# Kernel tuning notes

Hardware: AMD Instinct MI355X
Metric: run time of the kernel (lower is better)

The kernel has to match this reference:

```python
import jax, jax.numpy as jnp
import numpy as np

B, N, F_IN, F_OUT = 8, 2048, 64, 64
ALPHA = 0.2  # LeakyReLU negative slope


def setup_inputs() -> dict:
    key = jax.random.key(0)
    k_in, k_adj, k_w, k_a1, k_a2 = jax.random.split(key, 5)
    inp = jax.random.normal(k_in, (B, N, F_IN), dtype=jnp.float32)
    adj = (jax.random.uniform(k_adj, (B, N, N)) < 0.05).astype(jnp.float32)
    # xavier_uniform with gain=sqrt(2)
    def xavier(k, shape):
        fan_in, fan_out = shape[0], shape[1]
        bound = np.sqrt(2.0) * np.sqrt(6.0 / (fan_in + fan_out))
        return jax.random.uniform(k, shape, jnp.float32, -bound, bound)
    W = xavier(k_w, (F_IN, F_OUT))
    a1 = xavier(k_a1, (F_OUT, 1))
    a2 = xavier(k_a2, (F_OUT, 1))
    bias = jnp.full((N, F_OUT), 0.1, dtype=jnp.float32)
    return {"input": inp, "adj": adj, "W": W, "a1": a1, "a2": a2, "bias": bias}


def reference(input, adj, W, a1, a2, bias):
    # h: [B, N, F_OUT]
    h = jnp.einsum("bnf,fo->bno", input, W)
    f1 = h @ a1          # [B, N, 1]
    f2 = h @ a2          # [B, N, 1]
    e = jax.nn.leaky_relu(f1 + jnp.swapaxes(f2, 1, 2), negative_slope=ALPHA)  # [B, N, N]
    # NOTE: original multiplies adj elementwise (not -inf mask) and softmaxes over dim=1
    attention = jax.nn.softmax(adj * e, axis=1)
    h_prime = jnp.einsum("bij,bjo->bio", attention, h) + bias  # bias broadcasts over batch
    h_prime = h_prime + input  # in_features == out_features, no downsample
    return jax.nn.elu(h_prime)
```

## Files before the change

### kernel.cpp

```cpp
#include <hip/hip_runtime.h>
#include <cstdint>
#include <cstddef>

#define Bn 8
#define Nn 2048
#define Fn 64
#define ALPHA 0.2f

typedef __attribute__((ext_vector_type(8))) short  s8frag;
typedef __attribute__((ext_vector_type(4))) float  f4frag;

__device__ __forceinline__ float lrelu(float x) { return fmaxf(x, ALPHA * x); }
__device__ __forceinline__ float elu(float x)   { return x > 0.f ? x : __expf(x) - 1.f; }
__device__ __forceinline__ unsigned short bfr(float f) {
    unsigned u = __float_as_uint(f);
    u += 0x7fffu + ((u >> 16) & 1u);
    return (unsigned short)(u >> 16);
}

__global__ __launch_bounds__(256) void k1_h_f(
        const float* __restrict__ inp, const float* __restrict__ W,
        const float* __restrict__ a1, const float* __restrict__ a2,
        float* __restrict__ h, float* __restrict__ f1, float* __restrict__ f2) {
    __shared__ float Wl[Fn * Fn];
    __shared__ float inr[4 * Fn];
    int t = threadIdx.x;
    for (int k = t; k < Fn * Fn; k += 256) Wl[k] = W[k];
    size_t row0 = (size_t)blockIdx.x * 4;
    inr[t] = inp[row0 * Fn + t];
    __syncthreads();
    int r = t >> 6, o = t & 63;
    const float* irow = &inr[r * Fn];
    float acc = 0.f;
#pragma unroll
    for (int f = 0; f < Fn; ++f) acc = fmaf(irow[f], Wl[f * Fn + o], acc);
    size_t row = row0 + r;
    h[row * Fn + o] = acc;
    float p = acc * a1[o];
    float q = acc * a2[o];
#pragma unroll
    for (int off = 32; off > 0; off >>= 1) {
        p += __shfl_down(p, off, 64);
        q += __shfl_down(q, off, 64);
    }
    if (o == 0) { f1[row] = p; f2[row] = q; }
}

__global__ __launch_bounds__(256) void k1b_max(
        const float* __restrict__ f1, float* __restrict__ f1max) {
    int b = blockIdx.x, t = threadIdx.x;
    float m = -3.4e38f;
    for (int i = t; i < Nn; i += 256) m = fmaxf(m, f1[b * Nn + i]);
#pragma unroll
    for (int off = 32; off > 0; off >>= 1) m = fmaxf(m, __shfl_down(m, off, 64));
    __shared__ float sm[4];
    if ((t & 63) == 0) sm[t >> 6] = m;
    __syncthreads();
    if (t == 0) f1max[b] = fmaxf(fmaxf(sm[0], sm[1]), fmaxf(sm[2], sm[3]));
}

__global__ __launch_bounds__(512) void k2a_bits(
        const float* __restrict__ adj, const float* __restrict__ f1,
        const float* __restrict__ f2, const float* __restrict__ f1max_p,
        float* __restrict__ Dsum, unsigned char* __restrict__ bitsL) {
    int b = blockIdx.x;
    int cj = blockIdx.y;
    int j0 = cj * 256;
    int i0 = blockIdx.z * 128;
    int w = threadIdx.x >> 6, lane = threadIdx.x & 63;
    float f1max = f1max_p[b];
    float4 f2v = *(const float4*)&f2[b * Nn + j0 + 4 * lane];
    float Mf0 = fmaxf(lrelu(f1max + f2v.x), 0.f);
    float Mf1 = fmaxf(lrelu(f1max + f2v.y), 0.f);
    float Mf2 = fmaxf(lrelu(f1max + f2v.z), 0.f);
    float Mf3 = fmaxf(lrelu(f1max + f2v.w), 0.f);
    float s0 = 0.f, s1 = 0.f, s2 = 0.f, s3 = 0.f;
    const float* abase = adj + ((size_t)b * Nn) * Nn + j0 + 4 * lane;
    const float* f1b = f1 + b * Nn;
    int g = lane >> 1;
    int boff = (g & 3) * 8 + (g >> 2);
    bool evenlane = (lane & 1) == 0;
    size_t bbase = ((size_t)(b * 8 + cj) * Nn) * 32;

    for (int gi = 0; gi < 4; ++gi) {
        int r0 = i0 + w + 32 * gi;
        float4 av0 = *(const float4*)(abase + (size_t)(r0 +  0) * Nn);
        float4 av1 = *(const float4*)(abase + (size_t)(r0 +  8) * Nn);
        float4 av2 = *(const float4*)(abase + (size_t)(r0 + 16) * Nn);
        float4 av3 = *(const float4*)(abase + (size_t)(r0 + 24) * Nn);
        float fi0 = f1b[r0], fi1 = f1b[r0 + 8], fi2 = f1b[r0 + 16], fi3 = f1b[r0 + 24];
#define PROC(AV, FI, IROW)                                                     \
        {                                                                      \
            bool n0 = AV.x != 0.f, n1 = AV.y != 0.f,                           \
                 n2 = AV.z != 0.f, n3 = AV.w != 0.f;                           \
            s0 += __expf((n0 ? lrelu((FI) + f2v.x) : 0.f) - Mf0);              \
            s1 += __expf((n1 ? lrelu((FI) + f2v.y) : 0.f) - Mf1);              \
            s2 += __expf((n2 ? lrelu((FI) + f2v.z) : 0.f) - Mf2);              \
            s3 += __expf((n3 ? lrelu((FI) + f2v.w) : 0.f) - Mf3);              \
            unsigned nib = (unsigned)n0 | ((unsigned)n1 << 1) |                \
                           ((unsigned)n2 << 2) | ((unsigned)n3 << 3);          \
            unsigned other = __shfl_xor(nib, 1, 64);                           \
            if (evenlane)                                                      \
                bitsL[bbase + (size_t)(IROW) * 32 + boff] =                    \
                    (unsigned char)(nib | (other << 4));                       \
        }
        PROC(av0, fi0, r0 +  0)
        PROC(av1, fi1, r0 +  8)
        PROC(av2, fi2, r0 + 16)
        PROC(av3, fi3, r0 + 24)
#undef PROC
    }
    __shared__ float sred[8][256];
    sred[w][4 * lane + 0] = s0;
    sred[w][4 * lane + 1] = s1;
    sred[w][4 * lane + 2] = s2;
    sred[w][4 * lane + 3] = s3;
    __syncthreads();
    if (threadIdx.x < 256) {
        int c = threadIdx.x;
        float v = 0.f;
#pragma unroll
        for (int k = 0; k < 8; ++k) v += sred[k][c];
        atomicAdd(&Dsum[b * Nn + j0 + c], v);
    }
}

__global__ __launch_bounds__(256) void k2b_scale_T(
        const float* __restrict__ h, const float* __restrict__ Dsum,
        const float* __restrict__ f2, const float* __restrict__ f1max_p,
        unsigned short* __restrict__ hTs, float2* __restrict__ cf) {
    int b = blockIdx.x;
    int j0 = blockIdx.y * 64;
    int t = threadIdx.x;
    __shared__ float Lh[64][68];
    __shared__ float Rsh[64];
    if (t < 64) {
        int j = j0 + t;
        float f2j = f2[b * Nn + j];
        float Mf = fmaxf(lrelu(f1max_p[b] + f2j), 0.f);
        Rsh[t] = 1.f / Dsum[b * Nn + j];
        cf[b * Nn + j] = make_float2(f2j, Mf);
    }
#pragma unroll
    for (int q = 0; q < 4; ++q) {
        int fi = t + 256 * q;
        int jj = fi >> 4, oq = fi & 15;
        float4 v = *(const float4*)(h + ((size_t)(b * Nn + j0 + jj)) * Fn + oq * 4);
        *(float4*)&Lh[jj][oq * 4] = v;
    }
    __syncthreads();
    int o = t >> 2, jg = (t & 3) * 16;
    unsigned wbuf[8];
#pragma unroll
    for (int s2 = 0; s2 < 8; ++s2) {
        int j = jg + 2 * s2;
        unsigned lo16 = bfr(Lh[j][o] * Rsh[j]);
        unsigned hi16 = bfr(Lh[j + 1][o] * Rsh[j + 1]);
        wbuf[s2] = lo16 | (hi16 << 16);
    }
    unsigned short* dst = hTs + ((size_t)(b * Fn + o)) * Nn + j0 + jg;
    *(uint4*)dst       = make_uint4(wbuf[0], wbuf[1], wbuf[2], wbuf[3]);
    *(uint4*)(dst + 8) = make_uint4(wbuf[4], wbuf[5], wbuf[6], wbuf[7]);
}

__global__ __launch_bounds__(256) void k3_fused(
        const unsigned char* __restrict__ bitsL,
        const unsigned short* __restrict__ hTs,
        const float2* __restrict__ cf, const float* __restrict__ f1,
        const float* __restrict__ inp, const float* __restrict__ bias,
        float* __restrict__ out) {
    int b = blockIdx.x;
    int i0 = blockIdx.y * 64;
    int w = threadIdx.x >> 6, lane = threadIdx.x & 63;
    int m = lane & 15, kg = lane >> 4;
    int i = i0 + w * 16 + m;

    __shared__ float2 cfL[Nn];
    {
        const float4* src = (const float4*)(cf + (size_t)b * Nn);
        float4* dst = (float4*)cfL;
        for (int q = threadIdx.x; q < Nn / 2; q += 256) dst[q] = src[q];
    }
    uint2 pre[8];
#pragma unroll
    for (int jc = 0; jc < 8; ++jc)
        pre[jc] = *(const uint2*)(bitsL + ((size_t)(b * 8 + jc) * Nn + i) * 32 + kg * 8);
    float f1i = f1[b * Nn + i];
    __syncthreads();

    f4frag acc0 = {0.f,0.f,0.f,0.f}, acc1 = {0.f,0.f,0.f,0.f};
    f4frag acc2 = {0.f,0.f,0.f,0.f}, acc3 = {0.f,0.f,0.f,0.f};
    const unsigned short* Ab = hTs + (size_t)b * Fn * Nn + (size_t)m * Nn;

    for (int jc = 0; jc < 8; ++jc) {
        unsigned blo = pre[jc].x, bhi = pre[jc].y;
#pragma unroll 2
        for (int t = 0; t < 8; ++t) {
            unsigned bv = ((t < 4 ? blo : bhi) >> ((t & 3) * 8)) & 0xffu;
            int j = jc * 256 + t * 32 + kg * 8;
            const float2* cp = &cfL[j];
            s8frag bf;
#pragma unroll
            for (int r = 0; r < 8; ++r) {
                float2 c = cp[r];
                float l = lrelu(f1i + c.x);
                float arg = (((bv >> r) & 1u) ? l : 0.f) - c.y;
                bf[r] = (short)bfr(__expf(arg));
            }
            const unsigned short* Aj = Ab + j;
            s8frag a0 = *(const s8frag*)(Aj);
            s8frag a1 = *(const s8frag*)(Aj + 16 * Nn);
            s8frag a2 = *(const s8frag*)(Aj + 32 * Nn);
            s8frag a3 = *(const s8frag*)(Aj + 48 * Nn);
            acc0 = __builtin_amdgcn_mfma_f32_16x16x32_bf16(a0, bf, acc0, 0, 0, 0);
            acc1 = __builtin_amdgcn_mfma_f32_16x16x32_bf16(a1, bf, acc1, 0, 0, 0);
            acc2 = __builtin_amdgcn_mfma_f32_16x16x32_bf16(a2, bf, acc2, 0, 0, 0);
            acc3 = __builtin_amdgcn_mfma_f32_16x16x32_bf16(a3, bf, acc3, 0, 0, 0);
        }
    }
    size_t gbase = ((size_t)b * Nn + i) * Fn;
    int ob = kg * 4;
    f4frag accs[4] = {acc0, acc1, acc2, acc3};
#pragma unroll
    for (int ot = 0; ot < 4; ++ot) {
        int o = ot * 16 + ob;
        float4 iv  = *(const float4*)(inp + gbase + o);
        float4 bv4 = *(const float4*)(bias + (size_t)i * Fn + o);
        float4 r;
        r.x = elu(accs[ot][0] + iv.x + bv4.x);
        r.y = elu(accs[ot][1] + iv.y + bv4.y);
        r.z = elu(accs[ot][2] + iv.z + bv4.z);
        r.w = elu(accs[ot][3] + iv.w + bv4.w);
        *(float4*)(out + gbase + o) = r;
    }
}

extern "C" void kernel_launch(void* const* d_in, const int* in_sizes, int n_in,
                              void* d_out, int out_size, void* d_ws, size_t ws_size,
                              hipStream_t stream) {
    const float* inp  = (const float*)d_in[0];
    const float* adj  = (const float*)d_in[1];
    const float* W    = (const float*)d_in[2];
    const float* a1   = (const float*)d_in[3];
    const float* a2   = (const float*)d_in[4];
    const float* bias = (const float*)d_in[5];
    float* out = (float*)d_out;

    unsigned char* bitsL = (unsigned char*)d_ws;
    unsigned short* hTs  = (unsigned short*)(bitsL + (size_t)Bn * Nn * Nn / 8);
    float* h     = (float*)(hTs + (size_t)Bn * Fn * Nn);
    float* f1    = h + (size_t)Bn * Nn * Fn;
    float* f2    = f1 + (size_t)Bn * Nn;
    float* Dsum  = f2 + (size_t)Bn * Nn;
    float2* cf   = (float2*)(Dsum + (size_t)Bn * Nn);
    float* f1max = (float*)(cf + (size_t)Bn * Nn);

    hipMemsetAsync(Dsum, 0, (size_t)Bn * Nn * sizeof(float), stream);
    k1_h_f<<<Bn * Nn / 4, 256, 0, stream>>>(inp, W, a1, a2, h, f1, f2);
    k1b_max<<<Bn, 256, 0, stream>>>(f1, f1max);
    k2a_bits<<<dim3(Bn, 8, 16), 512, 0, stream>>>(adj, f1, f2, f1max, Dsum, bitsL);
    k2b_scale_T<<<dim3(Bn, Nn / 64), 256, 0, stream>>>(h, Dsum, f2, f1max, hTs, cf);
    k3_fused<<<dim3(Bn, Nn / 64), 256, 0, stream>>>(bitsL, hTs, cf, f1, inp, bias, out);
}
```

Measured before the change: 260.9 us.

## Factor exp of attention logits into precomputed products and split K across waves

The change rewrites exp(lrelu(f1+f2)-M) as a product of separately precomputed exponentials of f1 and f2, picked by the sign of the sum. Both the column-sum kernel and the fused attention-matmul kernel then use multiplies instead of a per-element exp. The fused kernel now gives each block 16 rows and splits the j dimension across its four waves, combining partial accumulators through shared memory, which gives four times as many blocks. The adjacency pass also software-prefetches the next row group. The factored products can overflow or underflow differently from the direct exp, and the cf buffer doubles to float4, which raises shared-memory use per block.

```diff
diff --git a/kernel.cpp b/kernel.cpp
--- a/kernel.cpp
+++ b/kernel.cpp
@@ -74,6 +74,10 @@
     float Mf1 = fmaxf(lrelu(f1max + f2v.y), 0.f);
     float Mf2 = fmaxf(lrelu(f1max + f2v.z), 0.f);
     float Mf3 = fmaxf(lrelu(f1max + f2v.w), 0.f);
+    float vh0 = __expf(f2v.x - Mf0), vp0 = __expf(ALPHA * f2v.x - Mf0), ez0 = __expf(-Mf0);
+    float vh1 = __expf(f2v.y - Mf1), vp1 = __expf(ALPHA * f2v.y - Mf1), ez1 = __expf(-Mf1);
+    float vh2 = __expf(f2v.z - Mf2), vp2 = __expf(ALPHA * f2v.z - Mf2), ez2 = __expf(-Mf2);
+    float vh3 = __expf(f2v.w - Mf3), vp3 = __expf(ALPHA * f2v.w - Mf3), ez3 = __expf(-Mf3);
     float s0 = 0.f, s1 = 0.f, s2 = 0.f, s3 = 0.f;
     const float* abase = adj + ((size_t)b * Nn) * Nn + j0 + 4 * lane;
     const float* f1b = f1 + b * Nn;
@@ -82,21 +86,41 @@
     bool evenlane = (lane & 1) == 0;
     size_t bbase = ((size_t)(b * 8 + cj) * Nn) * 32;
 
+    int rb = i0 + w;
+    float4 av0 = *(const float4*)(abase + (size_t)(rb +  0) * Nn);
+    float4 av1 = *(const float4*)(abase + (size_t)(rb +  8) * Nn);
+    float4 av2 = *(const float4*)(abase + (size_t)(rb + 16) * Nn);
+    float4 av3 = *(const float4*)(abase + (size_t)(rb + 24) * Nn);
+    float fi0 = f1b[rb], fi1 = f1b[rb + 8], fi2 = f1b[rb + 16], fi3 = f1b[rb + 24];
+
     for (int gi = 0; gi < 4; ++gi) {
-        int r0 = i0 + w + 32 * gi;
-        float4 av0 = *(const float4*)(abase + (size_t)(r0 +  0) * Nn);
-        float4 av1 = *(const float4*)(abase + (size_t)(r0 +  8) * Nn);
-        float4 av2 = *(const float4*)(abase + (size_t)(r0 + 16) * Nn);
-        float4 av3 = *(const float4*)(abase + (size_t)(r0 + 24) * Nn);
-        float fi0 = f1b[r0], fi1 = f1b[r0 + 8], fi2 = f1b[r0 + 16], fi3 = f1b[r0 + 24];
+        int rc = i0 + w + 32 * gi;
+        float4 nv0, nv1, nv2, nv3;
+        float nf0 = 0.f, nf1 = 0.f, nf2 = 0.f, nf3 = 0.f;
+        if (gi < 3) {
+            int rn = rc + 32;
+            nv0 = *(const float4*)(abase + (size_t)(rn +  0) * Nn);
+            nv1 = *(const float4*)(abase + (size_t)(rn +  8) * Nn);
+            nv2 = *(const float4*)(abase + (size_t)(rn + 16) * Nn);
+            nv3 = *(const float4*)(abase + (size_t)(rn + 24) * Nn);
+            nf0 = f1b[rn]; nf1 = f1b[rn + 8]; nf2 = f1b[rn + 16]; nf3 = f1b[rn + 24];
+        }
 #define PROC(AV, FI, IROW)                                                     \
         {                                                                      \
+            float u  = __expf(FI);                                             \
+            float up = __expf(ALPHA * (FI));                                   \
             bool n0 = AV.x != 0.f, n1 = AV.y != 0.f,                           \
                  n2 = AV.z != 0.f, n3 = AV.w != 0.f;                           \
-            s0 += __expf((n0 ? lrelu((FI) + f2v.x) : 0.f) - Mf0);              \
-            s1 += __expf((n1 ? lrelu((FI) + f2v.y) : 0.f) - Mf1);              \
-            s2 += __expf((n2 ? lrelu((FI) + f2v.z) : 0.f) - Mf2);              \
-            s3 += __expf((n3 ? lrelu((FI) + f2v.w) : 0.f) - Mf3);              \
+            float x0 = (FI) + f2v.x, x1 = (FI) + f2v.y,                        \
+                  x2 = (FI) + f2v.z, x3 = (FI) + f2v.w;                        \
+            float e0 = x0 > 0.f ? u * vh0 : up * vp0;                          \
+            float e1 = x1 > 0.f ? u * vh1 : up * vp1;                          \
+            float e2 = x2 > 0.f ? u * vh2 : up * vp2;                          \
+            float e3 = x3 > 0.f ? u * vh3 : up * vp3;                          \
+            s0 += n0 ? e0 : ez0;                                               \
+            s1 += n1 ? e1 : ez1;                                               \
+            s2 += n2 ? e2 : ez2;                                               \
+            s3 += n3 ? e3 : ez3;                                               \
             unsigned nib = (unsigned)n0 | ((unsigned)n1 << 1) |                \
                            ((unsigned)n2 << 2) | ((unsigned)n3 << 3);          \
             unsigned other = __shfl_xor(nib, 1, 64);                           \
@@ -104,11 +128,13 @@
                 bitsL[bbase + (size_t)(IROW) * 32 + boff] =                    \
                     (unsigned char)(nib | (other << 4));                       \
         }
-        PROC(av0, fi0, r0 +  0)
-        PROC(av1, fi1, r0 +  8)
-        PROC(av2, fi2, r0 + 16)
-        PROC(av3, fi3, r0 + 24)
+        PROC(av0, fi0, rc +  0)
+        PROC(av1, fi1, rc +  8)
+        PROC(av2, fi2, rc + 16)
+        PROC(av3, fi3, rc + 24)
 #undef PROC
+        av0 = nv0; av1 = nv1; av2 = nv2; av3 = nv3;
+        fi0 = nf0; fi1 = nf1; fi2 = nf2; fi3 = nf3;
     }
     __shared__ float sred[8][256];
     sred[w][4 * lane + 0] = s0;
@@ -128,7 +154,7 @@
 __global__ __launch_bounds__(256) void k2b_scale_T(
         const float* __restrict__ h, const float* __restrict__ Dsum,
         const float* __restrict__ f2, const float* __restrict__ f1max_p,
-        unsigned short* __restrict__ hTs, float2* __restrict__ cf) {
+        unsigned short* __restrict__ hTs, float4* __restrict__ cf4) {
     int b = blockIdx.x;
     int j0 = blockIdx.y * 64;
     int t = threadIdx.x;
@@ -139,7 +165,8 @@
         float f2j = f2[b * Nn + j];
         float Mf = fmaxf(lrelu(f1max_p[b] + f2j), 0.f);
         Rsh[t] = 1.f / Dsum[b * Nn + j];
-        cf[b * Nn + j] = make_float2(f2j, Mf);
+        cf4[b * Nn + j] = make_float4(f2j, __expf(f2j - Mf),
+                                      __expf(ALPHA * f2j - Mf), __expf(-Mf));
     }
 #pragma unroll
     for (int q = 0; q < 4; ++q) {
@@ -166,46 +193,46 @@
 __global__ __launch_bounds__(256) void k3_fused(
         const unsigned char* __restrict__ bitsL,
         const unsigned short* __restrict__ hTs,
-        const float2* __restrict__ cf, const float* __restrict__ f1,
+        const float4* __restrict__ cf4, const float* __restrict__ f1,
         const float* __restrict__ inp, const float* __restrict__ bias,
         float* __restrict__ out) {
     int b = blockIdx.x;
-    int i0 = blockIdx.y * 64;
+    int i0 = blockIdx.y * 16;
     int w = threadIdx.x >> 6, lane = threadIdx.x & 63;
     int m = lane & 15, kg = lane >> 4;
-    int i = i0 + w * 16 + m;
-
-    __shared__ float2 cfL[Nn];
+    int i = i0 + m;
+
+    __shared__ float4 shb[Nn];
     {
-        const float4* src = (const float4*)(cf + (size_t)b * Nn);
-        float4* dst = (float4*)cfL;
-        for (int q = threadIdx.x; q < Nn / 2; q += 256) dst[q] = src[q];
-    }
-    uint2 pre[8];
-#pragma unroll
-    for (int jc = 0; jc < 8; ++jc)
-        pre[jc] = *(const uint2*)(bitsL + ((size_t)(b * 8 + jc) * Nn + i) * 32 + kg * 8);
+        const float4* src = cf4 + (size_t)b * Nn;
+        for (int q = threadIdx.x; q < Nn; q += 256) shb[q] = src[q];
+    }
+    uint2 pre0 = *(const uint2*)(bitsL + ((size_t)(b * 8 + 2 * w) * Nn + i) * 32 + kg * 8);
+    uint2 pre1 = *(const uint2*)(bitsL + ((size_t)(b * 8 + 2 * w + 1) * Nn + i) * 32 + kg * 8);
     float f1i = f1[b * Nn + i];
+    float ui = __expf(f1i), upi = __expf(ALPHA * f1i);
     __syncthreads();
 
     f4frag acc0 = {0.f,0.f,0.f,0.f}, acc1 = {0.f,0.f,0.f,0.f};
     f4frag acc2 = {0.f,0.f,0.f,0.f}, acc3 = {0.f,0.f,0.f,0.f};
     const unsigned short* Ab = hTs + (size_t)b * Fn * Nn + (size_t)m * Nn;
 
-    for (int jc = 0; jc < 8; ++jc) {
-        unsigned blo = pre[jc].x, bhi = pre[jc].y;
+    for (int jcl = 0; jcl < 2; ++jcl) {
+        int jc = 2 * w + jcl;
+        unsigned blo = jcl ? pre1.x : pre0.x;
+        unsigned bhi = jcl ? pre1.y : pre0.y;
 #pragma unroll 2
         for (int t = 0; t < 8; ++t) {
             unsigned bv = ((t < 4 ? blo : bhi) >> ((t & 3) * 8)) & 0xffu;
             int j = jc * 256 + t * 32 + kg * 8;
-            const float2* cp = &cfL[j];
             s8frag bf;
 #pragma unroll
             for (int r = 0; r < 8; ++r) {
-                float2 c = cp[r];
-                float l = lrelu(f1i + c.x);
-                float arg = (((bv >> r) & 1u) ? l : 0.f) - c.y;
-                bf[r] = (short)bfr(__expf(arg));
+                float4 c = shb[j + r];
+                float x = f1i + c.x;
+                float uv = x > 0.f ? ui * c.y : upi * c.z;
+                float val = ((bv >> r) & 1u) ? uv : c.w;
+                bf[r] = (short)bfr(val);
             }
             const unsigned short* Aj = Ab + j;
             s8frag a0 = *(const s8frag*)(Aj);
@@ -218,21 +245,31 @@
             acc3 = __builtin_amdgcn_mfma_f32_16x16x32_bf16(a3, bf, acc3, 0, 0, 0);
         }
     }
-    size_t gbase = ((size_t)b * Nn + i) * Fn;
-    int ob = kg * 4;
+    __syncthreads();
     f4frag accs[4] = {acc0, acc1, acc2, acc3};
 #pragma unroll
-    for (int ot = 0; ot < 4; ++ot) {
-        int o = ot * 16 + ob;
-        float4 iv  = *(const float4*)(inp + gbase + o);
-        float4 bv4 = *(const float4*)(bias + (size_t)i * Fn + o);
-        float4 r;
-        r.x = elu(accs[ot][0] + iv.x + bv4.x);
-        r.y = elu(accs[ot][1] + iv.y + bv4.y);
-        r.z = elu(accs[ot][2] + iv.z + bv4.z);
-        r.w = elu(accs[ot][3] + iv.w + bv4.w);
-        *(float4*)(out + gbase + o) = r;
-    }
+    for (int ot = 0; ot < 4; ++ot)
+        shb[(w * 64 + lane) * 4 + ot] =
+            make_float4(accs[ot][0], accs[ot][1], accs[ot][2], accs[ot][3]);
+    __syncthreads();
+    int il = threadIdx.x & 15, oq = threadIdx.x >> 4;
+    int ot = oq >> 2, kg2 = oq & 3;
+    float4 v = make_float4(0.f, 0.f, 0.f, 0.f);
+#pragma unroll
+    for (int ww = 0; ww < 4; ++ww) {
+        float4 p = shb[(ww * 64 + kg2 * 16 + il) * 4 + ot];
+        v.x += p.x; v.y += p.y; v.z += p.z; v.w += p.w;
+    }
+    int o = oq * 4;
+    size_t gbase = ((size_t)b * Nn + i0 + il) * Fn + o;
+    float4 iv  = *(const float4*)(inp + gbase);
+    float4 bv4 = *(const float4*)(bias + (size_t)(i0 + il) * Fn + o);
+    float4 r;
+    r.x = elu(v.x + iv.x + bv4.x);
+    r.y = elu(v.y + iv.y + bv4.y);
+    r.z = elu(v.z + iv.z + bv4.z);
+    r.w = elu(v.w + iv.w + bv4.w);
+    *(float4*)(out + gbase) = r;
 }
 
 extern "C" void kernel_launch(void* const* d_in, const int* in_sizes, int n_in,
@@ -252,13 +289,13 @@
     float* f1    = h + (size_t)Bn * Nn * Fn;
     float* f2    = f1 + (size_t)Bn * Nn;
     float* Dsum  = f2 + (size_t)Bn * Nn;
-    float2* cf   = (float2*)(Dsum + (size_t)Bn * Nn);
-    float* f1max = (float*)(cf + (size_t)Bn * Nn);
+    float4* cf4  = (float4*)(Dsum + (size_t)Bn * Nn);
+    float* f1max = (float*)(cf4 + (size_t)Bn * Nn);
 
     hipMemsetAsync(Dsum, 0, (size_t)Bn * Nn * sizeof(float), stream);
     k1_h_f<<<Bn * Nn / 4, 256, 0, stream>>>(inp, W, a1, a2, h, f1, f2);
     k1b_max<<<Bn, 256, 0, stream>>>(f1, f1max);
     k2a_bits<<<dim3(Bn, 8, 16), 512, 0, stream>>>(adj, f1, f2, f1max, Dsum, bitsL);
-    k2b_scale_T<<<dim3(Bn, Nn / 64), 256, 0, stream>>>(h, Dsum, f2, f1max, hTs, cf);
-    k3_fused<<<dim3(Bn, Nn / 64), 256, 0, stream>>>(bitsL, hTs, cf, f1, inp, bias, out);
-}
+    k2b_scale_T<<<dim3(Bn, Nn / 64), 256, 0, stream>>>(h, Dsum, f2, f1max, hTs, cf4);
+    k3_fused<<<dim3(Bn, Nn / 16), 256, 0, stream>>>(bitsL, hTs, cf4, f1, inp, bias, out);
+}
```

Result: no change. 258.7 us (-0.8%).
